# Performance work log

Measured on AMD Instinct MI355X. Metric: run time of the kernel, lower is better.

The kernel has to match this reference:

```python
import jax, jax.numpy as jnp
import numpy as np

B, S, D, H = 2, 2048, 1024, 16
DK = D // H


def setup_inputs() -> dict:
    key = jax.random.key(0)
    ks = jax.random.split(key, 11)
    scale = 1.0 / np.sqrt(D)
    inp = {
        "q": jax.random.normal(ks[0], (B, S, D), jnp.float32),
        "k": jax.random.normal(ks[1], (B, S, D), jnp.float32),
        "v": jax.random.normal(ks[2], (B, S, D), jnp.float32),
        # causal mask, broadcastable to (B, H, S, S); 0 = masked
        "mask": jnp.tril(jnp.ones((S, S), jnp.int32))[None, None, :, :],
        "wq": jax.random.normal(ks[3], (D, D), jnp.float32) * scale,
        "bq": jax.random.normal(ks[4], (D,), jnp.float32) * scale,
        "wk": jax.random.normal(ks[5], (D, D), jnp.float32) * scale,
        "bk": jax.random.normal(ks[6], (D,), jnp.float32) * scale,
        "wv": jax.random.normal(ks[7], (D, D), jnp.float32) * scale,
        "bv": jax.random.normal(ks[8], (D,), jnp.float32) * scale,
        "wo": jax.random.normal(ks[9], (D, D), jnp.float32) * scale,
        "bo": jax.random.normal(ks[10], (D,), jnp.float32) * scale,
    }
    return inp


def reference(q, k, v, mask, wq, bq, wk, bk, wv, bv, wo, bo):
    # Linear projections (torch Linear: y = x @ W^T + b)
    Q = jnp.einsum('bsd,ed->bse', q, wq) + bq
    K = jnp.einsum('bsd,ed->bse', k, wk) + bk
    V = jnp.einsum('bsd,ed->bse', v, wv) + bv
    # split heads -> (B, H, S, d_k)
    Q = Q.reshape(B, S, H, DK).transpose(0, 2, 1, 3)
    K = K.reshape(B, S, H, DK).transpose(0, 2, 1, 3)
    V = V.reshape(B, S, H, DK).transpose(0, 2, 1, 3)
    # naive full-score attention, faithful to the source
    scores = jnp.einsum('bhqd,bhkd->bhqk', Q, K) / jnp.sqrt(jnp.float32(DK))
    scores = jnp.where(mask == 0, -jnp.inf, scores)
    attn = jax.nn.softmax(scores, axis=-1)
    out = jnp.einsum('bhqk,bhkd->bhqd', attn, V)
    # merge heads -> (B, S, D)
    out = out.transpose(0, 2, 1, 3).reshape(B, S, D)
    return jnp.einsum('bsd,ed->bse', out, wo) + bo
```

## Files before the change

### kernel.cpp

```cpp
#include <hip/hip_runtime.h>
#include <hip/hip_bf16.h>
#include <cstdint>

constexpr int Bc = 2, Sc = 2048, Dc = 1024, Hc = 16;
constexpr int Mtok = Bc * Sc;
constexpr float SCL = 0.125f * 1.44269504089f;

typedef __bf16 bf16;
typedef __bf16 bf16x4 __attribute__((ext_vector_type(4)));
typedef __bf16 bf16x8 __attribute__((ext_vector_type(8)));
typedef float  f32x4  __attribute__((ext_vector_type(4)));
typedef float  f32x16 __attribute__((ext_vector_type(16)));
typedef unsigned u32x4 __attribute__((ext_vector_type(4)));

__device__ __forceinline__ void gld_lds16(const bf16* g, bf16* l) {
  __builtin_amdgcn_global_load_lds(
      (__attribute__((address_space(1))) void*)(void*)g,
      (__attribute__((address_space(3))) void*)l, 16, 0, 0);
}

__device__ __forceinline__ bf16x8 ld8u(const bf16* p) {
  bf16x4 lo = *(const bf16x4*)p;
  bf16x4 hi = *(const bf16x4*)(p + 4);
  return __builtin_shufflevector(lo, hi, 0, 1, 2, 3, 4, 5, 6, 7);
}
__device__ __forceinline__ void st8u(bf16* p, bf16x8 v) {
  *(bf16x4*)p       = __builtin_shufflevector(v, v, 0, 1, 2, 3);
  *(bf16x4*)(p + 4) = __builtin_shufflevector(v, v, 4, 5, 6, 7);
}

__global__ __launch_bounds__(256) void convert_all(
    const float* __restrict__ q, const float* __restrict__ k,
    const float* __restrict__ v, const float* __restrict__ wq,
    const float* __restrict__ wk, const float* __restrict__ wv,
    const float* __restrict__ wo, bf16* __restrict__ ws)
{
  constexpr size_t NQ = (size_t)Mtok * Dc;
  constexpr size_t NW = (size_t)Dc * Dc;
  const size_t e = ((size_t)blockIdx.x * 256 + threadIdx.x) * 8;
  const float* src; bf16* dst;
  float scl = 1.0f;
  if (e < 3 * NQ) {
    src = (e < NQ) ? q + e : (e < 2 * NQ) ? k + (e - NQ) : v + (e - 2 * NQ);
    dst = ws + e;
  } else {
    const size_t w = e - 3 * NQ;
    const float* wsrc = (w < NW) ? wq : (w < 2 * NW) ? wk : (w < 3 * NW) ? wv : wo;
    if (w < NW) scl = SCL;
    src = wsrc + (w & (NW - 1));
    dst = ws + 5 * NQ + w;
  }
  f32x4 a = ((const f32x4*)src)[0];
  f32x4 b = ((const f32x4*)src)[1];
  bf16x8 t;
  t[0]=(bf16)(a[0]*scl); t[1]=(bf16)(a[1]*scl); t[2]=(bf16)(a[2]*scl); t[3]=(bf16)(a[3]*scl);
  t[4]=(bf16)(b[0]*scl); t[5]=(bf16)(b[1]*scl); t[6]=(bf16)(b[2]*scl); t[7]=(bf16)(b[7-7]*0 + b[3]*scl);
  *(bf16x8*)dst = t;
}

__global__ __launch_bounds__(256, 6) void gemm_qkv(
    const bf16* __restrict__ Aq, const bf16* __restrict__ Ak,
    const bf16* __restrict__ Av, const bf16* __restrict__ Wb,
    const float* __restrict__ bq, const float* __restrict__ bk,
    const float* __restrict__ bv,
    bf16* __restrict__ Yq, bf16* __restrict__ Yk, bf16* __restrict__ Vt)
{
  __shared__ __attribute__((aligned(16))) bf16 As[64 * 64];
  __shared__ __attribute__((aligned(16))) bf16 Bs[128 * 64];

  const int z = blockIdx.z;
  const bf16*  A    = (z == 0) ? Aq : (z == 1) ? Ak : Av;
  const bf16*  Wz   = Wb + (size_t)z * Dc * Dc;
  const float* bias = (z == 0) ? bq : (z == 1) ? bk : bv;

  const int m0 = blockIdx.x * 64, n0 = blockIdx.y * 128;
  const int tid = threadIdx.x, wave = tid >> 6, lane = tid & 63;
  const int quad = lane >> 4, l16 = lane & 15;
  const int swz = l16 & 7;
  const int sr  = lane >> 3;
  const int scol = ((lane & 7) ^ sr) * 8;

  f32x4 acc[4][2] = {};

  for (int k0 = 0; k0 < Dc; k0 += 64) {
#pragma unroll
    for (int j = 0; j < 2; ++j)
      gld_lds16(A + (size_t)(m0 + wave * 16 + j * 8 + sr) * Dc + k0 + scol,
                &As[(wave * 16 + j * 8) * 64]);
#pragma unroll
    for (int j = 0; j < 4; ++j)
      gld_lds16(Wz + (size_t)(n0 + wave * 32 + j * 8 + sr) * Dc + k0 + scol,
                &Bs[(wave * 32 + j * 8) * 64]);
    __syncthreads();
#pragma unroll
    for (int ks = 0; ks < 2; ++ks) {
      const int pc = ((ks * 4 + quad) ^ swz) * 8;
      bf16x8 af[4];
#pragma unroll
      for (int rt = 0; rt < 4; ++rt)
        af[rt] = *(const bf16x8*)&As[(rt * 16 + l16) * 64 + pc];
#pragma unroll
      for (int ct = 0; ct < 2; ++ct) {
        bf16x8 bfr = *(const bf16x8*)&Bs[(wave * 32 + ct * 16 + l16) * 64 + pc];
#pragma unroll
        for (int rt = 0; rt < 4; ++rt)
          acc[rt][ct] = __builtin_amdgcn_mfma_f32_16x16x32_bf16(af[rt], bfr, acc[rt][ct], 0, 0, 0);
      }
    }
    __syncthreads();
  }

  if (z < 2) {
    bf16* Y = (z == 0) ? Yq : Yk;
    const float bscl = (z == 0) ? SCL : 1.0f;
#pragma unroll
    for (int ct = 0; ct < 2; ++ct) {
      const int col = n0 + wave * 32 + ct * 16 + l16;
      const float bvv = bias[col] * bscl;
#pragma unroll
      for (int rt = 0; rt < 4; ++rt)
#pragma unroll
        for (int i = 0; i < 4; ++i) {
          const int row = m0 + rt * 16 + quad * 4 + i;
          Y[(size_t)row * Dc + col] = (bf16)(acc[rt][ct][i] + bvv);
        }
    }
  } else {
#pragma unroll
    for (int ct = 0; ct < 2; ++ct) {
      const int col = n0 + wave * 32 + ct * 16 + l16;
      const float bvv = bias[col];
#pragma unroll
      for (int rt = 0; rt < 4; ++rt) {
        const int row0 = m0 + rt * 16 + quad * 4;
        const int bb = row0 >> 11, s0 = row0 & 2047;
        bf16x4 pk;
#pragma unroll
        for (int i = 0; i < 4; ++i) pk[i] = (bf16)(acc[rt][ct][i] + bvv);
        *(bf16x4*)&Vt[((size_t)bb * Dc + col) * Sc + s0] = pk;
      }
    }
  }
}

__global__ __launch_bounds__(256, 4) void gemm_o(
    const bf16* __restrict__ A, const bf16* __restrict__ Wz,
    const float* __restrict__ bias, float* __restrict__ Y)
{
  __shared__ __attribute__((aligned(16))) bf16 As[64 * 64];
  __shared__ __attribute__((aligned(16))) bf16 Bs[64 * 64];

  const int m0 = blockIdx.x * 64, n0 = blockIdx.y * 64;
  const int tid = threadIdx.x, wave = tid >> 6, lane = tid & 63;
  const int quad = lane >> 4, l16 = lane & 15;
  const int swz = l16 & 7;
  const int sr  = lane >> 3;
  const int scol = ((lane & 7) ^ sr) * 8;

  f32x4 acc[4] = {};

  for (int k0 = 0; k0 < Dc; k0 += 64) {
#pragma unroll
    for (int j = 0; j < 2; ++j) {
      gld_lds16(A  + (size_t)(m0 + wave * 16 + j * 8 + sr) * Dc + k0 + scol,
                &As[(wave * 16 + j * 8) * 64]);
      gld_lds16(Wz + (size_t)(n0 + wave * 16 + j * 8 + sr) * Dc + k0 + scol,
                &Bs[(wave * 16 + j * 8) * 64]);
    }
    __syncthreads();
#pragma unroll
    for (int ks = 0; ks < 2; ++ks) {
      const int pc = ((ks * 4 + quad) ^ swz) * 8;
      bf16x8 bfr = *(const bf16x8*)&Bs[(wave * 16 + l16) * 64 + pc];
#pragma unroll
      for (int rt = 0; rt < 4; ++rt) {
        bf16x8 af = *(const bf16x8*)&As[(rt * 16 + l16) * 64 + pc];
        acc[rt] = __builtin_amdgcn_mfma_f32_16x16x32_bf16(af, bfr, acc[rt], 0, 0, 0);
      }
    }
    __syncthreads();
  }

  const int col = n0 + wave * 16 + l16;
  const float bvv = bias[col];
#pragma unroll
  for (int rt = 0; rt < 4; ++rt)
#pragma unroll
    for (int i = 0; i < 4; ++i) {
      const int row = m0 + rt * 16 + quad * 4 + i;
      Y[(size_t)row * Dc + col] = acc[rt][i] + bvv;
    }
}

template <bool AF32, bool BF32, bool OUTF32>
__global__ __launch_bounds__(256) void gemm128(
    const void* __restrict__ Av, const void* __restrict__ Bv,
    const float* __restrict__ bias, void* __restrict__ Yv,
    int M, int N, int K)
{
  __shared__ __attribute__((aligned(16))) bf16 As[2][128][40];
  __shared__ __attribute__((aligned(16))) bf16 Bs[2][128][40];

  const int m0 = blockIdx.x * 128, n0 = blockIdx.y * 128;
  const int tid = threadIdx.x, wave = tid >> 6, lane = tid & 63;
  const int quad = lane >> 4, l16 = lane & 15;
  const int rw = wave >> 1, cw = wave & 1;
  const int srow = tid >> 1, sc = (tid & 1) * 16;

  f32x4 acc[4][4] = {};

  auto load = [&](const void* P, bool f32, int r0, int k0, bf16x8& lo, bf16x8& hi) {
    if (f32) {
      const float* s = (const float*)P + (size_t)(r0 + srow) * K + k0 + sc;
      f32x4 a0 = ((const f32x4*)s)[0], a1 = ((const f32x4*)s)[1];
      f32x4 a2 = ((const f32x4*)s)[2], a3 = ((const f32x4*)s)[3];
      lo[0]=(bf16)a0[0]; lo[1]=(bf16)a0[1]; lo[2]=(bf16)a0[2]; lo[3]=(bf16)a0[3];
      lo[4]=(bf16)a1[0]; lo[5]=(bf16)a1[1]; lo[6]=(bf16)a1[2]; lo[7]=(bf16)a1[3];
      hi[0]=(bf16)a2[0]; hi[1]=(bf16)a2[1]; hi[2]=(bf16)a2[2]; hi[3]=(bf16)a2[3];
      hi[4]=(bf16)a3[0]; hi[5]=(bf16)a3[1]; hi[6]=(bf16)a3[2]; hi[7]=(bf16)a3[3];
    } else {
      const bf16* s = (const bf16*)P + (size_t)(r0 + srow) * K + k0 + sc;
      lo = ((const bf16x8*)s)[0]; hi = ((const bf16x8*)s)[1];
    }
  };

  bf16x8 alo, ahi, blo, bhi;
  load(Av, AF32, m0, 0, alo, ahi); load(Bv, BF32, n0, 0, blo, bhi);
  *(bf16x8*)&As[0][srow][sc] = alo; *(bf16x8*)&As[0][srow][sc + 8] = ahi;
  *(bf16x8*)&Bs[0][srow][sc] = blo; *(bf16x8*)&Bs[0][srow][sc + 8] = bhi;

  const int NIT = K >> 5;
  for (int it = 0; it < NIT; ++it) {
    __syncthreads();
    const int cur = it & 1;
    const bool pf = (it + 1) < NIT;
    if (pf) { load(Av, AF32, m0, (it+1)*32, alo, ahi); load(Bv, BF32, n0, (it+1)*32, blo, bhi); }

    bf16x8 af[4];
#pragma unroll
    for (int rt = 0; rt < 4; ++rt)
      af[rt] = *(const bf16x8*)&As[cur][rw * 64 + rt * 16 + l16][quad * 8];
#pragma unroll
    for (int ct = 0; ct < 4; ++ct) {
      bf16x8 bfr = *(const bf16x8*)&Bs[cur][cw * 64 + ct * 16 + l16][quad * 8];
#pragma unroll
      for (int rt = 0; rt < 4; ++rt)
        acc[rt][ct] = __builtin_amdgcn_mfma_f32_16x16x32_bf16(af[rt], bfr, acc[rt][ct], 0, 0, 0);
    }
    if (pf) {
      const int nxt = cur ^ 1;
      *(bf16x8*)&As[nxt][srow][sc] = alo; *(bf16x8*)&As[nxt][srow][sc + 8] = ahi;
      *(bf16x8*)&Bs[nxt][srow][sc] = blo; *(bf16x8*)&Bs[nxt][srow][sc + 8] = bhi;
    }
  }

#pragma unroll
  for (int ct = 0; ct < 4; ++ct) {
    const int col = n0 + cw * 64 + ct * 16 + l16;
    const float bvv = bias[col];
#pragma unroll
    for (int rt = 0; rt < 4; ++rt)
#pragma unroll
      for (int i = 0; i < 4; ++i) {
        const int row = m0 + rw * 64 + rt * 16 + quad * 4 + i;
        const float vv = acc[rt][ct][i] + bvv;
        if constexpr (OUTF32) ((float*)Yv)[(size_t)row * N + col] = vv;
        else                  ((bf16*)Yv)[(size_t)row * N + col] = (bf16)vv;
      }
  }
}

__global__ __launch_bounds__(256) void transpose_v(
    const bf16* __restrict__ in, bf16* __restrict__ out)
{
  __shared__ __attribute__((aligned(16))) bf16 tile[64][72];
  const int s0 = blockIdx.x * 64, d0 = blockIdx.y * 64, b = blockIdx.z;
  const int t = threadIdx.x, r = t >> 2, c = (t & 3) * 16;

  const bf16* src = in + (size_t)(b * Sc + s0 + r) * Dc + d0 + c;
  *(bf16x8*)&tile[r][c]     = ((const bf16x8*)src)[0];
  *(bf16x8*)&tile[r][c + 8] = ((const bf16x8*)src)[1];
  __syncthreads();

  bf16x8 t0, t1;
#pragma unroll
  for (int j = 0; j < 8; ++j) t0[j] = tile[c + j][r];
#pragma unroll
  for (int j = 0; j < 8; ++j) t1[j] = tile[c + 8 + j][r];
  bf16* dst = out + (size_t)(b * Dc + d0 + r) * Sc + s0 + c;
  ((bf16x8*)dst)[0] = t0;
  ((bf16x8*)dst)[1] = t1;
}

template <bool PRE>
__global__ __launch_bounds__(256, 4) void attn9(
    const bf16* __restrict__ Q, const bf16* __restrict__ K,
    const bf16* __restrict__ Vt, bf16* __restrict__ O)
{
  __shared__ __attribute__((aligned(16))) bf16 Ks[64][68];
  __shared__ __attribute__((aligned(16))) bf16 Vs[64][68];
  __shared__ float ls[4][32];

  const int bh = blockIdx.x, b = bh >> 4, h = bh & 15;
  const int t  = 15 - blockIdx.y;
  const int q0 = t * 128;
  const int nT = 2 * t + 2;

  const int tid = threadIdx.x, wave = tid >> 6, lane = tid & 63;
  const int l32 = lane & 31, hi = lane >> 5;
  const int hi4 = hi * 4, hi8 = hi * 8;
  const int nW = 2 * t + 1 + (wave >> 1);
  const int qg = q0 + wave * 32 + l32;

  const int row2 = tid >> 2;
  const int c8 = (tid & 3) * 2;
  const bf16* Kb = K  + ((size_t)(b * Sc + row2)) * Dc + h * 64 + c8 * 8;
  const bf16* Vb = Vt + ((size_t)(b * Dc + h * 64 + row2)) * Sc + c8 * 8;

  const bf16* qp = Q + (size_t)(b * Sc + qg) * Dc + h * 64;
  bf16x8 qf0 = *(const bf16x8*)(qp + 0 * 16 + hi8);
  bf16x8 qf1 = *(const bf16x8*)(qp + 1 * 16 + hi8);
  bf16x8 qf2 = *(const bf16x8*)(qp + 2 * 16 + hi8);
  bf16x8 qf3 = *(const bf16x8*)(qp + 3 * 16 + hi8);

  f32x16 oacc0 = {}, oacc1 = {};
  float lsum = 0.f;
  bf16x8 kr0, kr1, vr0, vr1;

  auto LOADS = [&](int kb) {
    const bf16* kp = Kb + (size_t)kb * 64 * Dc;
    kr0 = *(const bf16x8*)kp;
    kr1 = *(const bf16x8*)(kp + 8);
    const bf16* vp = Vb + kb * 64;
    vr0 = *(const bf16x8*)vp;
    vr1 = *(const bf16x8*)(vp + 8);
  };
  auto WRITES = [&]() {
    st8u(&Ks[row2][c8 * 8], kr0);
    st8u(&Ks[row2][c8 * 8 + 8], kr1);
    st8u(&Vs[row2][c8 * 8], vr0);
    st8u(&Vs[row2][c8 * 8 + 8], vr1);
  };

#define MHA_PK(R0, R1, DST)                                                   \
  do {                                                                        \
    float p0 = PRE ? __builtin_amdgcn_exp2f(s[R0])                            \
                   : __builtin_amdgcn_exp2f(s[R0] * SCL);                     \
    float p1 = PRE ? __builtin_amdgcn_exp2f(s[R1])                            \
                   : __builtin_amdgcn_exp2f(s[R1] * SCL);                     \
    if (dg) {                                                                 \
      p0 = ((((R0) & 3) + (((R0) >> 2) << 3) + hi4) <= kq) ? p0 : 0.f;        \
      p1 = ((((R1) & 3) + (((R1) >> 2) << 3) + hi4) <= kq) ? p1 : 0.f;        \
    }                                                                         \
    const bf16 b0 = (bf16)p0, b1 = (bf16)p1;                                  \
    lp += (float)b0 + (float)b1;                                              \
    DST = (unsigned)__builtin_bit_cast(unsigned short, b0) |                  \
          ((unsigned)__builtin_bit_cast(unsigned short, b1) << 16);           \
  } while (0)

  auto TILE = [&](int kb, bool dg) {
    const int kqb = qg - kb * 64;
#pragma unroll
    for (int blk = 0; blk < 2; ++blk) {
      f32x16 s = {};
      __builtin_amdgcn_s_setprio(1);
      {
        bf16x8 ak = ld8u(&Ks[blk * 32 + l32][0 * 16 + hi8]);
        s = __builtin_amdgcn_mfma_f32_32x32x16_bf16(ak, qf0, s, 0, 0, 0);
        ak = ld8u(&Ks[blk * 32 + l32][1 * 16 + hi8]);
        s = __builtin_amdgcn_mfma_f32_32x32x16_bf16(ak, qf1, s, 0, 0, 0);
        ak = ld8u(&Ks[blk * 32 + l32][2 * 16 + hi8]);
        s = __builtin_amdgcn_mfma_f32_32x32x16_bf16(ak, qf2, s, 0, 0, 0);
        ak = ld8u(&Ks[blk * 32 + l32][3 * 16 + hi8]);
        s = __builtin_amdgcn_mfma_f32_32x32x16_bf16(ak, qf3, s, 0, 0, 0);
      }
      __builtin_amdgcn_s_setprio(0);
      const int kq = kqb - blk * 32;
      float lp = 0.f;
      unsigned w0, w1, w2, w3, w4, w5, w6, w7;
      MHA_PK(0, 1, w0);   MHA_PK(2, 3, w1);
      MHA_PK(4, 5, w2);   MHA_PK(6, 7, w3);
      MHA_PK(8, 9, w4);   MHA_PK(10, 11, w5);
      MHA_PK(12, 13, w6); MHA_PK(14, 15, w7);
      lsum += lp;
      asm volatile("v_permlane32_swap_b32 %0, %1" : "+v"(w0), "+v"(w2));
      asm volatile("v_permlane32_swap_b32 %0, %1" : "+v"(w1), "+v"(w3));
      asm volatile("v_permlane32_swap_b32 %0, %1" : "+v"(w4), "+v"(w6));
      asm volatile("v_permlane32_swap_b32 %0, %1" : "+v"(w5), "+v"(w7));
      const u32x4 ua = {w0, w1, w2, w3};
      const u32x4 ub = {w4, w5, w6, w7};
      const bf16x8 f0 = __builtin_bit_cast(bf16x8, ua);
      const bf16x8 f1 = __builtin_bit_cast(bf16x8, ub);
      __builtin_amdgcn_s_setprio(1);
      {
        const int kc0 = (blk * 2 + 0) * 16 + hi8;
        const int kc1 = (blk * 2 + 1) * 16 + hi8;
        bf16x8 bv = ld8u(&Vs[0 * 32 + l32][kc0]);
        oacc0 = __builtin_amdgcn_mfma_f32_32x32x16_bf16(f0, bv, oacc0, 0, 0, 0);
        bv = ld8u(&Vs[1 * 32 + l32][kc0]);
        oacc1 = __builtin_amdgcn_mfma_f32_32x32x16_bf16(f0, bv, oacc1, 0, 0, 0);
        bv = ld8u(&Vs[0 * 32 + l32][kc1]);
        oacc0 = __builtin_amdgcn_mfma_f32_32x32x16_bf16(f1, bv, oacc0, 0, 0, 0);
        bv = ld8u(&Vs[1 * 32 + l32][kc1]);
        oacc1 = __builtin_amdgcn_mfma_f32_32x32x16_bf16(f1, bv, oacc1, 0, 0, 0);
      }
      __builtin_amdgcn_s_setprio(0);
    }
  };
#undef MHA_PK

  LOADS(0); WRITES();
  asm volatile("s_waitcnt lgkmcnt(0)" ::: "memory");
  __builtin_amdgcn_s_barrier();

  for (int i = 0; i < nT; ++i) {
    const bool pf = (i + 1) < nT;
    if (pf) LOADS(i + 1);
    if (i < nW) TILE(i, i == nW - 1);
    __builtin_amdgcn_s_barrier();
    if (pf) {
      WRITES();
      asm volatile("s_waitcnt lgkmcnt(0)" ::: "memory");
    }
    __builtin_amdgcn_s_barrier();
  }

  float la = lsum, lb = lsum;
  asm volatile("v_permlane32_swap_b32 %0, %1" : "+v"(la), "+v"(lb));
  const float rlt = 1.0f / (la + lb);
  if (hi == 0) ls[wave][l32] = rlt;
  asm volatile("s_waitcnt lgkmcnt(0)" ::: "memory");

#pragma unroll
  for (int r = 0; r < 16; ++r) {
    const int qr = (r & 3) + ((r >> 2) << 3) + hi4;
    const float rl = ls[wave][qr];
    const size_t orow = (size_t)(b * Sc + q0 + wave * 32 + qr) * Dc + h * 64;
    O[orow + 0 * 32 + l32] = (bf16)(oacc0[r] * rl);
    O[orow + 1 * 32 + l32] = (bf16)(oacc1[r] * rl);
  }
}

extern "C" void kernel_launch(void* const* d_in, const int* in_sizes, int n_in,
                              void* d_out, int out_size, void* d_ws, size_t ws_size,
                              hipStream_t stream)
{
  const float* q  = (const float*)d_in[0];
  const float* k  = (const float*)d_in[1];
  const float* v  = (const float*)d_in[2];
  const float* wq = (const float*)d_in[4];
  const float* bq = (const float*)d_in[5];
  const float* wk = (const float*)d_in[6];
  const float* bk = (const float*)d_in[7];
  const float* wv = (const float*)d_in[8];
  const float* bv = (const float*)d_in[9];
  const float* wo = (const float*)d_in[10];
  const float* bo = (const float*)d_in[11];
  float* out = (float*)d_out;

  constexpr size_t NQ = (size_t)Mtok * Dc;
  constexpr size_t NW = (size_t)Dc * Dc;
  bf16* W = (bf16*)d_ws;
  const dim3 ga(Hc * Bc, 16);
  const dim3 gt(Sc / 64, Dc / 64, Bc);

  const bool fancy = ws_size >= (size_t)(6 * NQ + 4 * NW) * 2;
  if (fancy) {
    bf16* xq = W;
    bf16* xk = W + NQ;
    bf16* xv = W + 2 * NQ;
    bf16* Qp = W + 3 * NQ;
    bf16* Kp = W + 4 * NQ;
    bf16* wb = W + 5 * NQ;
    bf16* Vt = W + 5 * NQ + 4 * NW;
    bf16* AO = W;

    convert_all<<<8192, 256, 0, stream>>>(q, k, v, wq, wk, wv, wo, W);
    gemm_qkv<<<dim3(Mtok / 64, Dc / 128, 3), 256, 0, stream>>>(
        xq, xk, xv, wb, bq, bk, bv, Qp, Kp, Vt);
    attn9<true><<<ga, 256, 0, stream>>>(Qp, Kp, Vt, AO);
    gemm_o<<<dim3(Mtok / 64, Dc / 64), 256, 0, stream>>>(AO, wb + 3 * NW, bo, out);
  } else {
    bf16* Qp = W;
    bf16* Kp = W + NQ;
    bf16* Vp = W + 2 * NQ;
    bf16* Vt = W + 3 * NQ;
    bf16* AO = W + 4 * NQ;
    const dim3 gg(Mtok / 128, Dc / 128);
    gemm128<true, true, false><<<gg, 256, 0, stream>>>(q, wq, bq, Qp, Mtok, Dc, Dc);
    gemm128<true, true, false><<<gg, 256, 0, stream>>>(k, wk, bk, Kp, Mtok, Dc, Dc);
    gemm128<true, true, false><<<gg, 256, 0, stream>>>(v, wv, bv, Vp, Mtok, Dc, Dc);
    transpose_v<<<gt, 256, 0, stream>>>(Vp, Vt);
    attn9<false><<<ga, 256, 0, stream>>>(Qp, Kp, Vt, AO);
    gemm128<false, true, true><<<gg, 256, 0, stream>>>(AO, wo, bo, out, Mtok, Dc, Dc);
  }
}
```

Before: 229.5 us.

## Split attention key range across two wave groups with LDS reduction

The attention kernel now runs 512 threads per block as two groups of four waves. Each group processes half of the causal key tiles for the same 128 query rows. Group 1 writes its partial output and row sums into LDS, which is unioned with the K/V buffers, and group 0 combines them and normalizes. Query-tile ordering is also reshuffled to interleave long and short blocks, and the row sum now accumulates fp32 probabilities instead of the bf16-rounded values. This halves the serial loop length per block, at the cost of more LDS, an extra reduction step and possibly lower occupancy.

```diff
diff --git a/kernel.cpp b/kernel.cpp
--- a/kernel.cpp
+++ b/kernel.cpp
@@ -54,7 +54,7 @@
   f32x4 b = ((const f32x4*)src)[1];
   bf16x8 t;
   t[0]=(bf16)(a[0]*scl); t[1]=(bf16)(a[1]*scl); t[2]=(bf16)(a[2]*scl); t[3]=(bf16)(a[3]*scl);
-  t[4]=(bf16)(b[0]*scl); t[5]=(bf16)(b[1]*scl); t[6]=(bf16)(b[2]*scl); t[7]=(bf16)(b[7-7]*0 + b[3]*scl);
+  t[4]=(bf16)(b[0]*scl); t[5]=(bf16)(b[1]*scl); t[6]=(bf16)(b[2]*scl); t[7]=(bf16)(b[3]*scl);
   *(bf16x8*)dst = t;
 }
 
@@ -293,27 +293,33 @@
 }
 
 template <bool PRE>
-__global__ __launch_bounds__(256, 4) void attn9(
+__global__ __launch_bounds__(512, 4) void attn10(
     const bf16* __restrict__ Q, const bf16* __restrict__ K,
     const bf16* __restrict__ Vt, bf16* __restrict__ O)
 {
-  __shared__ __attribute__((aligned(16))) bf16 Ks[64][68];
-  __shared__ __attribute__((aligned(16))) bf16 Vs[64][68];
+  union SMem {
+    struct { bf16 Ks[2][64][68]; bf16 Vs[2][64][68]; } m;
+    struct { float Ob[4][32][64]; float lb[4][32]; } x;
+  };
+  __shared__ __attribute__((aligned(16))) SMem sm;
   __shared__ float ls[4][32];
 
   const int bh = blockIdx.x, b = bh >> 4, h = bh & 15;
-  const int t  = 15 - blockIdx.y;
+  const int yy = blockIdx.y;
+  const int t  = (yy < 8) ? (15 - yy) : (yy - 8);
   const int q0 = t * 128;
-  const int nT = 2 * t + 2;
 
   const int tid = threadIdx.x, wave = tid >> 6, lane = tid & 63;
+  const int g = wave >> 2, w4 = wave & 3;
   const int l32 = lane & 31, hi = lane >> 5;
   const int hi4 = hi * 4, hi8 = hi * 8;
-  const int nW = 2 * t + 1 + (wave >> 1);
-  const int qg = q0 + wave * 32 + l32;
-
-  const int row2 = tid >> 2;
-  const int c8 = (tid & 3) * 2;
+  const int dmax = 2 * t + (w4 >> 1);
+  const int kbase = g ? (t + 1) : 0;
+  const int qg = q0 + w4 * 32 + l32;
+
+  const int lt = tid & 255;
+  const int row2 = lt >> 2;
+  const int c8 = (lt & 3) * 2;
   const bf16* Kb = K  + ((size_t)(b * Sc + row2)) * Dc + h * 64 + c8 * 8;
   const bf16* Vb = Vt + ((size_t)(b * Dc + h * 64 + row2)) * Sc + c8 * 8;
 
@@ -336,10 +342,10 @@
     vr1 = *(const bf16x8*)(vp + 8);
   };
   auto WRITES = [&]() {
-    st8u(&Ks[row2][c8 * 8], kr0);
-    st8u(&Ks[row2][c8 * 8 + 8], kr1);
-    st8u(&Vs[row2][c8 * 8], vr0);
-    st8u(&Vs[row2][c8 * 8 + 8], vr1);
+    st8u(&sm.m.Ks[g][row2][c8 * 8], kr0);
+    st8u(&sm.m.Ks[g][row2][c8 * 8 + 8], kr1);
+    st8u(&sm.m.Vs[g][row2][c8 * 8], vr0);
+    st8u(&sm.m.Vs[g][row2][c8 * 8 + 8], vr1);
   };
 
 #define MHA_PK(R0, R1, DST)                                                   \
@@ -352,8 +358,8 @@
       p0 = ((((R0) & 3) + (((R0) >> 2) << 3) + hi4) <= kq) ? p0 : 0.f;        \
       p1 = ((((R1) & 3) + (((R1) >> 2) << 3) + hi4) <= kq) ? p1 : 0.f;        \
     }                                                                         \
+    lp += p0 + p1;                                                            \
     const bf16 b0 = (bf16)p0, b1 = (bf16)p1;                                  \
-    lp += (float)b0 + (float)b1;                                              \
     DST = (unsigned)__builtin_bit_cast(unsigned short, b0) |                  \
           ((unsigned)__builtin_bit_cast(unsigned short, b1) << 16);           \
   } while (0)
@@ -365,43 +371,43 @@
       f32x16 s = {};
       __builtin_amdgcn_s_setprio(1);
       {
-        bf16x8 ak = ld8u(&Ks[blk * 32 + l32][0 * 16 + hi8]);
+        bf16x8 ak = ld8u(&sm.m.Ks[g][blk * 32 + l32][0 * 16 + hi8]);
         s = __builtin_amdgcn_mfma_f32_32x32x16_bf16(ak, qf0, s, 0, 0, 0);
-        ak = ld8u(&Ks[blk * 32 + l32][1 * 16 + hi8]);
+        ak = ld8u(&sm.m.Ks[g][blk * 32 + l32][1 * 16 + hi8]);
         s = __builtin_amdgcn_mfma_f32_32x32x16_bf16(ak, qf1, s, 0, 0, 0);
-        ak = ld8u(&Ks[blk * 32 + l32][2 * 16 + hi8]);
+        ak = ld8u(&sm.m.Ks[g][blk * 32 + l32][2 * 16 + hi8]);
         s = __builtin_amdgcn_mfma_f32_32x32x16_bf16(ak, qf2, s, 0, 0, 0);
-        ak = ld8u(&Ks[blk * 32 + l32][3 * 16 + hi8]);
+        ak = ld8u(&sm.m.Ks[g][blk * 32 + l32][3 * 16 + hi8]);
         s = __builtin_amdgcn_mfma_f32_32x32x16_bf16(ak, qf3, s, 0, 0, 0);
       }
       __builtin_amdgcn_s_setprio(0);
       const int kq = kqb - blk * 32;
       float lp = 0.f;
-      unsigned w0, w1, w2, w3, w4, w5, w6, w7;
+      unsigned w0, w1, w2, w3, w4r, w5, w6, w7;
       MHA_PK(0, 1, w0);   MHA_PK(2, 3, w1);
       MHA_PK(4, 5, w2);   MHA_PK(6, 7, w3);
-      MHA_PK(8, 9, w4);   MHA_PK(10, 11, w5);
+      MHA_PK(8, 9, w4r);  MHA_PK(10, 11, w5);
       MHA_PK(12, 13, w6); MHA_PK(14, 15, w7);
       lsum += lp;
       asm volatile("v_permlane32_swap_b32 %0, %1" : "+v"(w0), "+v"(w2));
       asm volatile("v_permlane32_swap_b32 %0, %1" : "+v"(w1), "+v"(w3));
-      asm volatile("v_permlane32_swap_b32 %0, %1" : "+v"(w4), "+v"(w6));
+      asm volatile("v_permlane32_swap_b32 %0, %1" : "+v"(w4r), "+v"(w6));
       asm volatile("v_permlane32_swap_b32 %0, %1" : "+v"(w5), "+v"(w7));
       const u32x4 ua = {w0, w1, w2, w3};
-      const u32x4 ub = {w4, w5, w6, w7};
+      const u32x4 ub = {w4r, w5, w6, w7};
       const bf16x8 f0 = __builtin_bit_cast(bf16x8, ua);
       const bf16x8 f1 = __builtin_bit_cast(bf16x8, ub);
       __builtin_amdgcn_s_setprio(1);
       {
         const int kc0 = (blk * 2 + 0) * 16 + hi8;
         const int kc1 = (blk * 2 + 1) * 16 + hi8;
-        bf16x8 bv = ld8u(&Vs[0 * 32 + l32][kc0]);
+        bf16x8 bv = ld8u(&sm.m.Vs[g][0 * 32 + l32][kc0]);
         oacc0 = __builtin_amdgcn_mfma_f32_32x32x16_bf16(f0, bv, oacc0, 0, 0, 0);
-        bv = ld8u(&Vs[1 * 32 + l32][kc0]);
+        bv = ld8u(&sm.m.Vs[g][1 * 32 + l32][kc0]);
         oacc1 = __builtin_amdgcn_mfma_f32_32x32x16_bf16(f0, bv, oacc1, 0, 0, 0);
-        bv = ld8u(&Vs[0 * 32 + l32][kc1]);
+        bv = ld8u(&sm.m.Vs[g][0 * 32 + l32][kc1]);
         oacc0 = __builtin_amdgcn_mfma_f32_32x32x16_bf16(f1, bv, oacc0, 0, 0, 0);
-        bv = ld8u(&Vs[1 * 32 + l32][kc1]);
+        bv = ld8u(&sm.m.Vs[g][1 * 32 + l32][kc1]);
         oacc1 = __builtin_amdgcn_mfma_f32_32x32x16_bf16(f1, bv, oacc1, 0, 0, 0);
       }
       __builtin_amdgcn_s_setprio(0);
@@ -409,14 +415,15 @@
   };
 #undef MHA_PK
 
-  LOADS(0); WRITES();
+  LOADS(kbase); WRITES();
   asm volatile("s_waitcnt lgkmcnt(0)" ::: "memory");
   __builtin_amdgcn_s_barrier();
 
-  for (int i = 0; i < nT; ++i) {
-    const bool pf = (i + 1) < nT;
-    if (pf) LOADS(i + 1);
-    if (i < nW) TILE(i, i == nW - 1);
+  for (int i = 0; i <= t; ++i) {
+    const bool pf = i < t;
+    if (pf) LOADS(kbase + i + 1);
+    const int kbc = kbase + i;
+    if (kbc <= dmax) TILE(kbc, kbc == dmax);
     __builtin_amdgcn_s_barrier();
     if (pf) {
       WRITES();
@@ -425,19 +432,33 @@
     __builtin_amdgcn_s_barrier();
   }
 
-  float la = lsum, lb = lsum;
-  asm volatile("v_permlane32_swap_b32 %0, %1" : "+v"(la), "+v"(lb));
-  const float rlt = 1.0f / (la + lb);
-  if (hi == 0) ls[wave][l32] = rlt;
+  float la = lsum, lb2 = lsum;
+  asm volatile("v_permlane32_swap_b32 %0, %1" : "+v"(la), "+v"(lb2));
+  const float ltot = la + lb2;
+
+  if (g == 1) {
+#pragma unroll
+    for (int r = 0; r < 16; ++r) {
+      const int qr = (r & 3) + ((r >> 2) << 3) + hi4;
+      sm.x.Ob[w4][qr][l32]      = oacc0[r];
+      sm.x.Ob[w4][qr][32 + l32] = oacc1[r];
+    }
+    if (hi == 0) sm.x.lb[w4][l32] = ltot;
+  }
   asm volatile("s_waitcnt lgkmcnt(0)" ::: "memory");
-
-#pragma unroll
-  for (int r = 0; r < 16; ++r) {
-    const int qr = (r & 3) + ((r >> 2) << 3) + hi4;
-    const float rl = ls[wave][qr];
-    const size_t orow = (size_t)(b * Sc + q0 + wave * 32 + qr) * Dc + h * 64;
-    O[orow + 0 * 32 + l32] = (bf16)(oacc0[r] * rl);
-    O[orow + 1 * 32 + l32] = (bf16)(oacc1[r] * rl);
+  __builtin_amdgcn_s_barrier();
+  if (g == 0) {
+    const float rlt = 1.0f / (ltot + sm.x.lb[w4][l32]);
+    if (hi == 0) ls[w4][l32] = rlt;
+    asm volatile("s_waitcnt lgkmcnt(0)" ::: "memory");
+#pragma unroll
+    for (int r = 0; r < 16; ++r) {
+      const int qr = (r & 3) + ((r >> 2) << 3) + hi4;
+      const float rl = ls[w4][qr];
+      const size_t orow = (size_t)(b * Sc + q0 + w4 * 32 + qr) * Dc + h * 64;
+      O[orow + l32]      = (bf16)((oacc0[r] + sm.x.Ob[w4][qr][l32]) * rl);
+      O[orow + 32 + l32] = (bf16)((oacc1[r] + sm.x.Ob[w4][qr][32 + l32]) * rl);
+    }
   }
 }
 
@@ -478,7 +499,7 @@
     convert_all<<<8192, 256, 0, stream>>>(q, k, v, wq, wk, wv, wo, W);
     gemm_qkv<<<dim3(Mtok / 64, Dc / 128, 3), 256, 0, stream>>>(
         xq, xk, xv, wb, bq, bk, bv, Qp, Kp, Vt);
-    attn9<true><<<ga, 256, 0, stream>>>(Qp, Kp, Vt, AO);
+    attn10<true><<<ga, 512, 0, stream>>>(Qp, Kp, Vt, AO);
     gemm_o<<<dim3(Mtok / 64, Dc / 64), 256, 0, stream>>>(AO, wb + 3 * NW, bo, out);
   } else {
     bf16* Qp = W;
@@ -491,7 +512,7 @@
     gemm128<true, true, false><<<gg, 256, 0, stream>>>(k, wk, bk, Kp, Mtok, Dc, Dc);
     gemm128<true, true, false><<<gg, 256, 0, stream>>>(v, wv, bv, Vp, Mtok, Dc, Dc);
     transpose_v<<<gt, 256, 0, stream>>>(Vp, Vt);
-    attn9<false><<<ga, 256, 0, stream>>>(Qp, Kp, Vt, AO);
+    attn10<false><<<ga, 512, 0, stream>>>(Qp, Kp, Vt, AO);
     gemm128<false, true, true><<<gg, 256, 0, stream>>>(AO, wo, bo, out, Mtok, Dc, Dc);
   }
 }
```

After: 313.4 us. 1.37x slower.
